# Optimization experiments

Hardware: AMD Instinct MI355X
Metric: run time of the kernel (lower is better)

Reference implementation:

```python
import jax, jax.numpy as jnp
import numpy as np

B, H, W, Q, E, M, K, WIN = 4, 192, 192, 160, 96, 96, 4, 7
NO_ELECTRON_WEIGHT = 0.1


def _bce_logits(x, z):
    # binary_cross_entropy_with_logits, elementwise: softplus(x) - x*z
    return jnp.logaddexp(0.0, x) - x * z


def setup_inputs() -> dict:
    key = jax.random.key(0)
    ks = jax.random.split(key, 11)
    is_electron_logit = jax.random.normal(ks[0], (B * Q,), jnp.float32)
    true_segmap = jax.random.uniform(ks[1], (B, H, W, E), jnp.float32)
    binary_mask_logits = jax.random.normal(ks[2], (B, H, W, Q), jnp.float32)
    portion_logits = jax.random.normal(ks[3], (B, H, W, Q), jnp.float32)
    # keep incidence points away from borders so the 7x7 window stays in-bounds
    incidence_points = jax.random.uniform(ks[4], (B, E, 2), jnp.float32) * (H - 8) + 4.0
    positions = jax.random.uniform(ks[5], (B, Q, 2), jnp.float32) * H
    a = jax.random.normal(ks[6], (B, Q, 3), jnp.float32)
    l00 = jax.nn.softplus(a[..., 0]) + 0.1
    l11 = jax.nn.softplus(a[..., 2]) + 0.1
    l10 = 0.5 * a[..., 1]
    zero = jnp.zeros_like(l00)
    chol = jnp.stack([jnp.stack([l00, zero], -1), jnp.stack([l10, l11], -1)], -2)  # [B,Q,2,2] lower-tri
    occupancy_logits = jax.random.normal(ks[7], (B, H, W, K), jnp.float32)
    occupancy_true = jax.random.randint(ks[8], (B, H, W), 0, K, jnp.int32)
    qkeys = jax.random.split(ks[9], B)
    matched_q = jnp.stack([jax.random.permutation(k, Q)[:M] for k in qkeys]).astype(jnp.int32)
    ekeys = jax.random.split(ks[10], B)
    matched_e = jnp.stack([jax.random.permutation(k, E) for k in ekeys]).astype(jnp.int32)
    return dict(is_electron_logit=is_electron_logit, true_segmap=true_segmap,
                binary_mask_logits=binary_mask_logits, portion_logits=portion_logits,
                incidence_points=incidence_points, positions=positions, chol=chol,
                occupancy_logits=occupancy_logits, occupancy_true=occupancy_true,
                matched_q=matched_q, matched_e=matched_e)


def reference(is_electron_logit, true_segmap, binary_mask_logits, portion_logits,
              incidence_points, positions, chol, occupancy_logits, occupancy_true,
              matched_q, matched_e):
    # ---- class loss (weighted BCE over flat per-query logits) ----
    labels = jnp.zeros((B * Q,), is_electron_logit.dtype)
    glob = (jnp.arange(B)[:, None] * Q + matched_q).reshape(-1)
    labels = labels.at[glob].set(1.0)
    weights = jnp.where(labels > 0, 1.0, NO_ELECTRON_WEIGHT).astype(is_electron_logit.dtype)
    class_loss = jnp.mean(weights * _bce_logits(is_electron_logit, labels))

    # ---- reorder segmentation maps to matched order (_reorder_segmentation_map) ----
    true_r = jnp.take_along_axis(true_segmap, matched_e[:, None, None, :], axis=3)        # [B,H,W,M]
    bin_r = jnp.take_along_axis(binary_mask_logits, matched_q[:, None, None, :], axis=3)  # [B,H,W,M]
    por_r = jnp.take_along_axis(portion_logits, matched_q[:, None, None, :], axis=3)      # [B,H,W,M]

    # ---- mask BCE on 7x7 windows around floor(matched incidence point) ----
    pts_r = jnp.take_along_axis(incidence_points, matched_e[..., None], axis=1)  # [B,M,2]
    pix = jnp.floor(pts_r).astype(jnp.int32)
    half = WIN // 2
    dr = jnp.arange(-half, half + 1)
    rows = pix[..., 0][:, :, None, None] + dr[None, None, :, None]  # [B,M,7,1]
    cols = pix[..., 1][:, :, None, None] + dr[None, None, None, :]  # [B,M,1,7]
    bi = jnp.arange(B)[:, None, None, None]
    mi = jnp.arange(M)[None, :, None, None]
    tv = true_r[bi, rows, cols, mi]  # [B,M,7,7]
    lg = bin_r[bi, rows, cols, mi]
    bce_loss = jnp.mean(_bce_logits(lg, tv))

    # ---- dice loss (softmax over matched-electron dim) ----
    portion = jax.nn.softmax(por_r, axis=-1)
    num = jnp.sum(2.0 * true_r * portion, axis=(1, 2, 3))
    den = jnp.sum(true_r + portion, axis=(1, 2, 3))
    dice_loss = jnp.mean(1.0 - (num + 1.0) / (den + 1.0))

    # ---- distance NLL (2D MVN with lower-tri scale) ----
    centers_r = jnp.take_along_axis(positions, matched_q[..., None], axis=1)       # [B,M,2]
    chol_r = jnp.take_along_axis(chol, matched_q[..., None, None], axis=1)         # [B,M,2,2]
    d = pts_r - centers_r
    z0 = d[..., 0] / chol_r[..., 0, 0]
    z1 = (d[..., 1] - chol_r[..., 1, 0] * z0) / chol_r[..., 1, 1]
    nll = 0.5 * (z0 * z0 + z1 * z1) + jnp.log(2.0 * jnp.pi) \
          + jnp.log(chol_r[..., 0, 0]) + jnp.log(chol_r[..., 1, 1])
    nll = jnp.where(jnp.isinf(nll), 1e7, nll)
    nll_loss = jnp.mean(nll)

    # ---- occupancy loss (per-pixel electron-count cross-entropy) ----
    logp = jax.nn.log_softmax(occupancy_logits, axis=-1)
    occ_loss = -jnp.mean(jnp.take_along_axis(logp, occupancy_true[..., None], axis=-1))

    # loss_weights all 1.0 (defaults); dot(weights, terms)
    return class_loss + bce_loss + dice_loss + nll_loss + occ_loss
```

## Files before the change

### kernel.cpp

```cpp
#include <hip/hip_runtime.h>
#include <math.h>

#define B_ 4
#define H_ 192
#define W_ 192
#define Q_ 160
#define E_ 96
#define M_ 96
#define HW_ (H_ * W_)
#define NPIX_ (B_ * HW_)
#define TPIX 8
#define NTILE 18
#define NBUF 4
#define TILE_B 8192
#define NDICE 1024
#define NSMALL 962
#define NBUCKET 64
#define WS_NUM0 4
#define WS_TS0  260
#define WS_TOTAL 516

__device__ __forceinline__ void stage16(const void* g, void* l) {
    __builtin_amdgcn_global_load_lds(
        (const __attribute__((address_space(1))) void*)g,
        (__attribute__((address_space(3))) void*)l, 16, 0, 0);
}

template <int CTRL, int RMASK>
__device__ __forceinline__ float dpp_add_step(float x) {
    int v = __builtin_amdgcn_update_dpp(0, __float_as_int(x), CTRL, RMASK, 0xF, false);
    return x + __int_as_float(v);
}
__device__ __forceinline__ float wave_sum63(float x) {
    x = dpp_add_step<0x111, 0xF>(x);
    x = dpp_add_step<0x112, 0xF>(x);
    x = dpp_add_step<0x114, 0xF>(x);
    x = dpp_add_step<0x118, 0xF>(x);
    x = dpp_add_step<0x142, 0xA>(x);
    x = dpp_add_step<0x143, 0xC>(x);
    return x;
}

__device__ __forceinline__ float waveSumAll(float v) {
    for (int m = 32; m > 0; m >>= 1) v += __shfl_xor(v, m, 64);
    return v;
}

__device__ __forceinline__ float softplusf(float x) {
    return fmaxf(x, 0.f) + log1pf(__expf(-fabsf(x)));
}

__global__ __launch_bounds__(256) void fused_kernel(
    const float* __restrict__ logit,
    const float* __restrict__ trueseg,
    const float* __restrict__ binlog,
    const float* __restrict__ por,
    const float* __restrict__ inc,
    const float* __restrict__ pos,
    const float* __restrict__ chol,
    const float* __restrict__ occlog,
    const int* __restrict__ occtrue,
    const int* __restrict__ mqall,
    const int* __restrict__ meall,
    float* __restrict__ ws)
{
    __shared__ float tilebuf[NBUF * TILE_B / 4];
    const int tid  = threadIdx.x;
    const int lane = tid & 63;
    const int wid  = tid >> 6;
    const int blk  = blockIdx.x;

    if (blk < NDICE) {
        const int b = blk >> 8;
        const int slot = blk & 255;
        const bool hi = lane < 32;
        const int l31 = lane & 31;
        const int* mq = mqall + b * M_;
        const int* me = meall + b * M_;
        const int mqa = mq[lane];
        const int mea = me[lane];
        const int mqb = mq[64 + l31];
        const int meb = me[64 + l31];
        const float m1 = hi ? 1.f : 0.f;

        const char* porb = (const char*)(por + (size_t)b * HW_ * Q_);
        const char* trb  = (const char*)(trueseg + (size_t)b * HW_ * E_);

        asm volatile("s_waitcnt vmcnt(0)" ::: "memory");

        float an = 0.f;
        float at = 0.f;

        #define STAGE(t_) do {                                                 \
            const int p0_ = (slot + (t_) * 256) * TPIX;                        \
            const char* gp_ = porb + (size_t)p0_ * (Q_ * 4);                   \
            const char* gt_ = trb  + (size_t)p0_ * (E_ * 4);                   \
            char* dst_ = (char*)tilebuf + ((t_) & (NBUF - 1)) * TILE_B;        \
            const int o0_ = wid * 1024;                                        \
            const char* s0_ = (o0_ < 5120) ? (gp_ + o0_) : (gt_ + o0_ - 5120); \
            stage16(s0_ + lane * 16, dst_ + o0_);                              \
            const int o1_ = o0_ + 4096;                                        \
            const char* s1_ = (o1_ < 5120) ? (gp_ + o1_) : (gt_ + o1_ - 5120); \
            stage16(s1_ + lane * 16, dst_ + o1_);                              \
        } while (0)

        #define COMP(t_) do {                                                  \
            const float* pl_ = tilebuf + ((t_) & (NBUF - 1)) * (TILE_B / 4);   \
            const float* tl_ = pl_ + TPIX * Q_;                                \
            _Pragma("unroll")                                                  \
            for (int k = 0; k < 2; ++k) {                                      \
                const int pix_ = wid * 2 + k;                                  \
                float p0v_ = pl_[pix_ * Q_ + mqa];                             \
                float t0_  = tl_[pix_ * E_ + mea];                             \
                float p1_  = pl_[pix_ * Q_ + mqb];                             \
                float t1_  = tl_[pix_ * E_ + meb];                             \
                float e0_ = __expf(p0v_);                                      \
                float e1_ = __expf(p1_) * m1;                                  \
                float s_  = wave_sum63(e0_ + e1_);                             \
                float se_ = wave_sum63(fmaf(t1_, e1_, t0_ * e0_));             \
                an += __fdividef(se_, s_);                                     \
                at += fmaf(t1_, m1, t0_);                                      \
            }                                                                  \
        } while (0)

        STAGE(0); STAGE(1); STAGE(2);

        #pragma unroll 4
        for (int t = 0; t < NTILE - 2; ++t) {
            asm volatile("s_waitcnt vmcnt(4)" ::: "memory");
            asm volatile("s_waitcnt lgkmcnt(0)" ::: "memory");
            __builtin_amdgcn_s_barrier();
            __builtin_amdgcn_sched_barrier(0);
            if (t + 3 < NTILE) STAGE(t + 3);
            COMP(t);
        }
        asm volatile("s_waitcnt vmcnt(2)" ::: "memory");
        asm volatile("s_waitcnt lgkmcnt(0)" ::: "memory");
        __builtin_amdgcn_s_barrier();
        __builtin_amdgcn_sched_barrier(0);
        COMP(NTILE - 2);
        asm volatile("s_waitcnt vmcnt(0)" ::: "memory");
        asm volatile("s_waitcnt lgkmcnt(0)" ::: "memory");
        __builtin_amdgcn_s_barrier();
        __builtin_amdgcn_sched_barrier(0);
        COMP(NTILE - 1);

        #undef STAGE
        #undef COMP

        float atr = wave_sum63(at);
        if (lane == 63) {
            int bucket = blk & (NBUCKET - 1);
            atomicAdd(&ws[WS_NUM0 + bucket * 4 + b], 2.f * an);
            atomicAdd(&ws[WS_TS0  + bucket * 4 + b], atr);
        }
    } else {
        float* lab = tilebuf;
        const int s = blk - NDICE;
        float acc = 0.f;
        if (s == 0) {
            for (int i = tid; i < B_ * Q_; i += 256) lab[i] = 0.f;
            __syncthreads();
            for (int i = tid; i < B_ * M_; i += 256) {
                int b = i / M_;
                lab[b * Q_ + mqall[i]] = 1.f;
            }
            __syncthreads();
            for (int i = tid; i < B_ * Q_; i += 256) {
                float x = logit[i];
                float z = lab[i];
                float w = z > 0.f ? 1.f : 0.1f;
                acc += w * (softplusf(x) - x * z);
            }
            float wsum = wave_sum63(acc);
            if (lane == 63) atomicAdd(&ws[0], wsum);
        } else if (s == 1) {
            for (int i = tid; i < B_ * M_; i += 256) {
                int b = i / M_;
                int qi = mqall[i];
                int ei = meall[i];
                float px = inc[(b * E_ + ei) * 2 + 0];
                float py = inc[(b * E_ + ei) * 2 + 1];
                float cx = pos[(b * Q_ + qi) * 2 + 0];
                float cy = pos[(b * Q_ + qi) * 2 + 1];
                const float* ch = chol + (size_t)(b * Q_ + qi) * 4;
                float l00 = ch[0], l10 = ch[2], l11 = ch[3];
                float d0 = px - cx, d1 = py - cy;
                float z0 = d0 / l00;
                float z1 = (d1 - l10 * z0) / l11;
                float nll = 0.5f * (z0 * z0 + z1 * z1) + 1.837877066409345f
                            + logf(l00) + logf(l11);
                if (isinf(nll)) nll = 1e7f;
                acc += nll;
            }
            float wsum = wave_sum63(acc);
            if (lane == 63) atomicAdd(&ws[2], wsum);
        } else if (s < 386) {
            int idx = s - 2;
            int b = idx / M_;
            int ei = meall[idx];
            int qi = mqall[idx];
            float px = inc[(b * E_ + ei) * 2 + 0];
            float py = inc[(b * E_ + ei) * 2 + 1];
            int r0 = (int)floorf(px) - 3;
            int c0 = (int)floorf(py) - 3;
            if (tid < 49) {
                int rr = r0 + tid / 7;
                int cc = c0 + tid % 7;
                size_t pix = ((size_t)b * H_ + rr) * W_ + cc;
                float tv = trueseg[pix * E_ + ei];
                float lg = binlog[pix * Q_ + qi];
                acc = softplusf(lg) - lg * tv;
            }
            if (wid == 0) {
                float wsum = wave_sum63(acc);
                if (lane == 63) atomicAdd(&ws[1], wsum);
            }
        } else {
            int p = (s - 386) * 256 + tid;
            if (p < NPIX_) {
                float4 v = *(const float4*)(occlog + (size_t)p * 4);
                int lb = occtrue[p];
                float m = fmaxf(fmaxf(v.x, v.y), fmaxf(v.z, v.w));
                float lse = m + __logf(__expf(v.x - m) + __expf(v.y - m) +
                                       __expf(v.z - m) + __expf(v.w - m));
                float xs = lb == 0 ? v.x : (lb == 1 ? v.y : (lb == 2 ? v.z : v.w));
                acc = lse - xs;
            }
            float wsum = wave_sum63(acc);
            if (lane == 63) atomicAdd(&ws[3], wsum);
        }
    }
}

__global__ __launch_bounds__(64) void final_kernel(const float* __restrict__ ws,
                                                   float* __restrict__ out)
{
    const int lane = threadIdx.x;
    float n[B_], t[B_];
    for (int b = 0; b < B_; ++b) {
        n[b] = waveSumAll(ws[WS_NUM0 + lane * 4 + b]);
        t[b] = waveSumAll(ws[WS_TS0  + lane * 4 + b]);
    }
    if (lane == 0) {
        float class_l = ws[0] * (1.f / (B_ * Q_));
        float bce_l   = ws[1] * (1.f / (B_ * M_ * 49));
        float nll_l   = ws[2] * (1.f / (B_ * M_));
        float occ_l   = ws[3] * (1.f / NPIX_);
        float dice = 0.f;
        for (int b = 0; b < B_; ++b)
            dice += 1.f - (n[b] + 1.f) / (t[b] + (float)HW_ + 1.f);
        dice *= (1.f / B_);
        out[0] = class_l + bce_l + nll_l + occ_l + dice;
    }
}

extern "C" void kernel_launch(void* const* d_in, const int* in_sizes, int n_in,
                              void* d_out, int out_size, void* d_ws, size_t ws_size,
                              hipStream_t stream) {
    const float* logit   = (const float*)d_in[0];
    const float* trueseg = (const float*)d_in[1];
    const float* binlog  = (const float*)d_in[2];
    const float* por     = (const float*)d_in[3];
    const float* inc     = (const float*)d_in[4];
    const float* pos     = (const float*)d_in[5];
    const float* chol    = (const float*)d_in[6];
    const float* occlog  = (const float*)d_in[7];
    const int*   occtrue = (const int*)d_in[8];
    const int*   mq      = (const int*)d_in[9];
    const int*   me      = (const int*)d_in[10];
    float* out = (float*)d_out;
    float* ws  = (float*)d_ws;

    (void)hipMemsetAsync(d_ws, 0, WS_TOTAL * sizeof(float), stream);

    hipLaunchKernelGGL(fused_kernel, dim3(NDICE + NSMALL), dim3(256), 0, stream,
                       logit, trueseg, binlog, por, inc, pos, chol, occlog, occtrue,
                       mq, me, ws);
    hipLaunchKernelGGL(final_kernel, dim3(1), dim3(64), 0, stream, ws, out);
}
```

Before: 262.7 us.

## Give each wave a private double-buffered LDS tile and drop block barriers

The dice loop changes from block-shared 4-deep tiles of 8 pixels to per-wave 2-deep tiles of 4 pixels each, with 16 pixels per block per step and 9 steps instead of 18. Each wave now stages its own pixels' portion and true-segment rows into its own LDS region. This lets the workgroup-wide s_barrier calls go, so waves run independently instead of stalling on the slowest wave every tile. The cost is a shallower prefetch (two buffers instead of four), so memory latency is less hidden per wave. Correctness now depends on each wave's own vmcnt and lgkmcnt waits guarding reuse of its buffer.

```diff
diff --git a/kernel.cpp b/kernel.cpp
--- a/kernel.cpp
+++ b/kernel.cpp
@@ -9,10 +9,8 @@
 #define M_ 96
 #define HW_ (H_ * W_)
 #define NPIX_ (B_ * HW_)
-#define TPIX 8
-#define NTILE 18
-#define NBUF 4
-#define TILE_B 8192
+#define NTILE 9
+#define WTILE_B 4096
 #define NDICE 1024
 #define NSMALL 962
 #define NBUCKET 64
@@ -64,7 +62,7 @@
     const int* __restrict__ meall,
     float* __restrict__ ws)
 {
-    __shared__ float tilebuf[NBUF * TILE_B / 4];
+    __shared__ float tilebuf[4 * 2 * WTILE_B / 4];
     const int tid  = threadIdx.x;
     const int lane = tid & 63;
     const int wid  = tid >> 6;
@@ -88,32 +86,34 @@
 
         asm volatile("s_waitcnt vmcnt(0)" ::: "memory");
 
+        char* wbase = (char*)tilebuf + wid * (2 * WTILE_B);
+
         float an = 0.f;
         float at = 0.f;
 
         #define STAGE(t_) do {                                                 \
-            const int p0_ = (slot + (t_) * 256) * TPIX;                        \
-            const char* gp_ = porb + (size_t)p0_ * (Q_ * 4);                   \
-            const char* gt_ = trb  + (size_t)p0_ * (E_ * 4);                   \
-            char* dst_ = (char*)tilebuf + ((t_) & (NBUF - 1)) * TILE_B;        \
-            const int o0_ = wid * 1024;                                        \
-            const char* s0_ = (o0_ < 5120) ? (gp_ + o0_) : (gt_ + o0_ - 5120); \
-            stage16(s0_ + lane * 16, dst_ + o0_);                              \
-            const int o1_ = o0_ + 4096;                                        \
-            const char* s1_ = (o1_ < 5120) ? (gp_ + o1_) : (gt_ + o1_ - 5120); \
-            stage16(s1_ + lane * 16, dst_ + o1_);                              \
+            const int p0_ = (slot + (t_) * 256) * 16 + wid * 4;                \
+            const char* gp_ = porb + (size_t)p0_ * 640;                        \
+            const char* gt_ = trb  + (size_t)p0_ * 384;                        \
+            char* dst_ = wbase + ((t_) & 1) * WTILE_B;                         \
+            _Pragma("unroll")                                                  \
+            for (int i_ = 0; i_ < 4; ++i_) {                                   \
+                const int off_ = i_ * 1024 + lane * 16;                        \
+                const char* s_ = (off_ < 2560) ? (gp_ + off_)                  \
+                                               : (gt_ + (off_ - 2560));        \
+                stage16(s_, dst_ + i_ * 1024);                                 \
+            }                                                                  \
         } while (0)
 
         #define COMP(t_) do {                                                  \
-            const float* pl_ = tilebuf + ((t_) & (NBUF - 1)) * (TILE_B / 4);   \
-            const float* tl_ = pl_ + TPIX * Q_;                                \
+            const float* pl_ = (const float*)(wbase + ((t_) & 1) * WTILE_B);   \
+            const float* tl_ = pl_ + 640;                                      \
             _Pragma("unroll")                                                  \
-            for (int k = 0; k < 2; ++k) {                                      \
-                const int pix_ = wid * 2 + k;                                  \
-                float p0v_ = pl_[pix_ * Q_ + mqa];                             \
-                float t0_  = tl_[pix_ * E_ + mea];                             \
-                float p1_  = pl_[pix_ * Q_ + mqb];                             \
-                float t1_  = tl_[pix_ * E_ + meb];                             \
+            for (int k_ = 0; k_ < 4; ++k_) {                                   \
+                float p0v_ = pl_[k_ * Q_ + mqa];                               \
+                float t0_  = tl_[k_ * E_ + mea];                               \
+                float p1_  = pl_[k_ * Q_ + mqb];                               \
+                float t1_  = tl_[k_ * E_ + meb];                               \
                 float e0_ = __expf(p0v_);                                      \
                 float e1_ = __expf(p1_) * m1;                                  \
                 float s_  = wave_sum63(e0_ + e1_);                             \
@@ -123,26 +123,17 @@
             }                                                                  \
         } while (0)
 
-        STAGE(0); STAGE(1); STAGE(2);
-
-        #pragma unroll 4
+        STAGE(0); STAGE(1);
+
         for (int t = 0; t < NTILE - 2; ++t) {
             asm volatile("s_waitcnt vmcnt(4)" ::: "memory");
+            COMP(t);
             asm volatile("s_waitcnt lgkmcnt(0)" ::: "memory");
-            __builtin_amdgcn_s_barrier();
-            __builtin_amdgcn_sched_barrier(0);
-            if (t + 3 < NTILE) STAGE(t + 3);
-            COMP(t);
+            STAGE(t + 2);
         }
-        asm volatile("s_waitcnt vmcnt(2)" ::: "memory");
-        asm volatile("s_waitcnt lgkmcnt(0)" ::: "memory");
-        __builtin_amdgcn_s_barrier();
-        __builtin_amdgcn_sched_barrier(0);
+        asm volatile("s_waitcnt vmcnt(4)" ::: "memory");
         COMP(NTILE - 2);
         asm volatile("s_waitcnt vmcnt(0)" ::: "memory");
-        asm volatile("s_waitcnt lgkmcnt(0)" ::: "memory");
-        __builtin_amdgcn_s_barrier();
-        __builtin_amdgcn_sched_barrier(0);
         COMP(NTILE - 1);
 
         #undef STAGE
```

After: 262.9 us. About the same (+0.1%).
